# Kernel optimization log

Measured on AMD Instinct MI355X. Metric: run time of the kernel, lower is better.

## Reference

```python
import jax, jax.numpy as jnp
import numpy as np

N = 100000
E = 1600000
IN_C = 128
HID_C = 32
HEADS = 4
OUT_C = 64
NUM_CLASSES = 2
NUM_GRAPHS = 64
NEG_SLOPE = 0.2  # PyG GATConv default leaky_relu slope


def _segment_softmax(logits, seg, num_segments):
    # logits: [E, H], seg: [E] destination node ids
    m = jax.ops.segment_max(logits, seg, num_segments=num_segments)
    m = jnp.where(jnp.isfinite(m), m, 0.0)
    e = jnp.exp(logits - m[seg])
    s = jax.ops.segment_sum(e, seg, num_segments=num_segments)
    return e / (s[seg] + 1e-16)


def _gat_conv(x, src, dst, W, att_src, att_dst, bias, heads, ch, concat):
    n = x.shape[0]
    h = (x @ W).reshape(n, heads, ch)                 # [N, H, C]
    a_src = jnp.sum(h * att_src, axis=-1)             # [N, H]
    a_dst = jnp.sum(h * att_dst, axis=-1)             # [N, H]
    alpha = jax.nn.leaky_relu(a_src[src] + a_dst[dst], NEG_SLOPE)  # [E, H]
    alpha = _segment_softmax(alpha, dst, n)
    msg = h[src] * alpha[:, :, None]                  # [E, H, C]
    out = jax.ops.segment_sum(msg, dst, num_segments=n)  # [N, H, C]
    out = out.reshape(n, heads * ch) if concat else out.mean(axis=1)
    return out + bias


def setup_inputs() -> dict:
    key = jax.random.key(0)
    ks = jax.random.split(key, 12)
    x = jax.random.normal(ks[0], (N, IN_C), dtype=jnp.float32)
    edge_index = jax.random.randint(ks[1], (2, E), 0, N, dtype=jnp.int32)
    batch = jnp.sort(jax.random.randint(ks[2], (N,), 0, NUM_GRAPHS, dtype=jnp.int32))
    s1 = 1.0 / np.sqrt(IN_C)
    W1 = jax.random.uniform(ks[3], (IN_C, HEADS * HID_C), minval=-s1, maxval=s1, dtype=jnp.float32)
    att_src1 = jax.random.normal(ks[4], (HEADS, HID_C), dtype=jnp.float32) * 0.1
    att_dst1 = jax.random.normal(ks[5], (HEADS, HID_C), dtype=jnp.float32) * 0.1
    b1 = jnp.zeros((HEADS * HID_C,), dtype=jnp.float32)
    s2 = 1.0 / np.sqrt(HEADS * HID_C)
    W2 = jax.random.uniform(ks[6], (HEADS * HID_C, OUT_C), minval=-s2, maxval=s2, dtype=jnp.float32)
    att_src2 = jax.random.normal(ks[7], (1, OUT_C), dtype=jnp.float32) * 0.1
    att_dst2 = jax.random.normal(ks[8], (1, OUT_C), dtype=jnp.float32) * 0.1
    b2 = jnp.zeros((OUT_C,), dtype=jnp.float32)
    sc = 1.0 / np.sqrt(OUT_C)
    Wc = jax.random.uniform(ks[9], (OUT_C, NUM_CLASSES), minval=-sc, maxval=sc, dtype=jnp.float32)
    bc = jnp.zeros((NUM_CLASSES,), dtype=jnp.float32)
    return {"x": x, "edge_index": edge_index, "batch": batch,
            "W1": W1, "att_src1": att_src1, "att_dst1": att_dst1, "b1": b1,
            "W2": W2, "att_src2": att_src2, "att_dst2": att_dst2, "b2": b2,
            "Wc": Wc, "bc": bc}


def reference(x, edge_index, batch, W1, att_src1, att_dst1, b1,
              W2, att_src2, att_dst2, b2, Wc, bc):
    # PyG GATConv adds self-loops by default
    loops = jnp.arange(N, dtype=edge_index.dtype)
    src = jnp.concatenate([edge_index[0], loops])
    dst = jnp.concatenate([edge_index[1], loops])
    # eval mode: dropout is identity
    h = _gat_conv(x, src, dst, W1, att_src1, att_dst1, b1, HEADS, HID_C, True)
    h = jax.nn.elu(h)
    h = _gat_conv(h, src, dst, W2, att_src2, att_dst2, b2, 1, OUT_C, False)
    h = jax.nn.elu(h)
    # global mean pool over graphs
    sums = jax.ops.segment_sum(h, batch, num_segments=NUM_GRAPHS)
    cnts = jax.ops.segment_sum(jnp.ones((N, 1), h.dtype), batch, num_segments=NUM_GRAPHS)
    pooled = sums / jnp.maximum(cnts, 1.0)
    return pooled @ Wc + bc
```

## Files before the change

kernel.cpp:

```cpp
#include <hip/hip_runtime.h>
#include <math.h>


typedef __attribute__((ext_vector_type(8))) short bf16x8;
typedef __attribute__((ext_vector_type(4))) float f32x4;

__device__ __forceinline__ unsigned f2bf_rne(float x){
  unsigned u = __float_as_uint(x);
  return (u + 0x7fffu + ((u >> 16) & 1u)) >> 16;
}
__device__ __forceinline__ unsigned pk_bf2(float a, float b){
  return f2bf_rne(a) | (f2bf_rne(b) << 16);
}
__device__ __forceinline__ void unpack8(uint4 q, float* f){
  f[0] = __uint_as_float(q.x << 16);
  f[1] = __uint_as_float(q.x & 0xffff0000u);
  f[2] = __uint_as_float(q.y << 16);
  f[3] = __uint_as_float(q.y & 0xffff0000u);
  f[4] = __uint_as_float(q.z << 16);
  f[5] = __uint_as_float(q.z & 0xffff0000u);
  f[6] = __uint_as_float(q.w << 16);
  f[7] = __uint_as_float(q.w & 0xffff0000u);
}


#define CHUNKE 2048

__global__ __launch_bounds__(256) void k_bucketcount(
    const int* __restrict__ dst, int* __restrict__ bcnt, int e, int NB)
{
  __shared__ int hcnt[512];
  const int tid = threadIdx.x;
  for (int b = tid; b < 512; b += 256) hcnt[b] = 0;
  __syncthreads();
  const int lo = blockIdx.x * CHUNKE;
  const int hi = min(lo + CHUNKE, e);
  for (int i = lo + tid; i < hi; i += 256)
    atomicAdd(&hcnt[dst[i] >> 8], 1);
  __syncthreads();
  for (int b = tid; b < NB; b += 256)
    if (hcnt[b]) atomicAdd(&bcnt[b], hcnt[b]);
}

__global__ __launch_bounds__(512) void k_bucketscan(
    const int* __restrict__ bcnt, int* __restrict__ bbase,
    int* __restrict__ cur, int* __restrict__ off, int e, int n, int NB)
{
  __shared__ int sh[512];
  const int t = threadIdx.x;
  int v = (t < NB) ? bcnt[t] : 0;
  sh[t] = v;
  __syncthreads();
  for (int o = 1; o < 512; o <<= 1){
    int x = (t >= o) ? sh[t - o] : 0;
    __syncthreads();
    sh[t] += x;
    __syncthreads();
  }
  if (t < NB){
    int excl = sh[t] - v;
    bbase[t] = excl;
    cur[t]   = excl;
  }
  if (t == 0) off[n] = e;
}

__global__ __launch_bounds__(256) void k_partition(
    const int* __restrict__ src, const int* __restrict__ dst,
    int* __restrict__ cur, unsigned* __restrict__ packed, int e, int NB)
{
  __shared__ int hcnt[512];
  __shared__ int hbase[512];
  const int tid = threadIdx.x;
  for (int b = tid; b < 512; b += 256) hcnt[b] = 0;
  __syncthreads();
  const int lo = blockIdx.x * CHUNKE;
  const int hi = min(lo + CHUNKE, e);
  for (int i = lo + tid; i < hi; i += 256)
    atomicAdd(&hcnt[dst[i] >> 8], 1);
  __syncthreads();
  for (int b = tid; b < NB; b += 256){
    int c = hcnt[b];
    hbase[b] = c ? atomicAdd(&cur[b], c) : 0;
    hcnt[b] = 0;
  }
  __syncthreads();
  for (int i = lo + tid; i < hi; i += 256){
    int d = dst[i];
    int b = d >> 8;
    int p = hbase[b] + atomicAdd(&hcnt[b], 1);
    packed[p] = (unsigned)src[i] | ((unsigned)(d & 255) << 17);
  }
}

__global__ __launch_bounds__(256) void k_bucketbuild(
    const unsigned* __restrict__ packed, const int* __restrict__ bbase,
    const int* __restrict__ bcnt, int* __restrict__ off,
    int* __restrict__ csr, int n)
{
  __shared__ int lcnt[256];
  __shared__ int loff[256];
  const int b    = blockIdx.x;
  const int tid  = threadIdx.x;
  const int seg0 = bbase[b];
  const int scnt = bcnt[b];

  lcnt[tid] = 0;
  __syncthreads();
  for (int i = tid; i < scnt; i += 256)
    atomicAdd(&lcnt[packed[seg0 + i] >> 17], 1);
  __syncthreads();
  int v = lcnt[tid];
  loff[tid] = v;
  __syncthreads();
  for (int o = 1; o < 256; o <<= 1){
    int x = (tid >= o) ? loff[tid - o] : 0;
    __syncthreads();
    loff[tid] += x;
    __syncthreads();
  }
  int excl = loff[tid] - v;
  __syncthreads();
  loff[tid] = excl;
  lcnt[tid] = 0;
  int d = (b << 8) + tid;
  if (d < n) off[d] = seg0 + excl;
  __syncthreads();
  for (int i = tid; i < scnt; i += 256){
    unsigned rec = packed[seg0 + i];
    int doff = rec >> 17;
    int s    = rec & 0x1FFFF;
    int p    = atomicAdd(&lcnt[doff], 1);
    csr[seg0 + loff[doff] + p] = s;
  }
}


template<int OUTC, int HEADS, bool XBF16, typename XT>
__global__ __launch_bounds__(256) void k_gemm_mfma(
    const XT* __restrict__ X, const float* __restrict__ W,
    const float* __restrict__ att_s, const float* __restrict__ att_d,
    unsigned short* __restrict__ H, float* __restrict__ ASRC,
    float* __restrict__ ADST, int n)
{
  constexpr int K  = 128;
  constexpr int KC = 32;
  constexpr int CT = OUTC / 16;
  constexpr int RT = 16 / CT;
  constexpr int WROWS = RT * 16;
  constexpr int BROWS = WROWS * 4;

  __shared__ unsigned short Bs[OUTC][K + 8];
  __shared__ unsigned short As[BROWS][KC + 8];

  const int tid   = threadIdx.x;
  const int lane  = tid & 63;
  const int c15   = lane & 15;
  const int quad  = lane >> 4;
  const int warow = (tid >> 6) * WROWS;
  const int row0  = blockIdx.x * BROWS;

  f32x4 acc[CT][RT];
  #pragma unroll
  for (int ct = 0; ct < CT; ++ct)
    #pragma unroll
    for (int t = 0; t < RT; ++t)
      #pragma unroll
      for (int r = 0; r < 4; ++r) acc[ct][t][r] = 0.f;

  for (int idx = tid; idx < K * OUTC / 4; idx += 256){
    int k  = idx / (OUTC / 4);
    int c4 = (idx % (OUTC / 4)) * 4;
    float4 v = *(const float4*)&W[(size_t)k * OUTC + c4];
    Bs[c4 + 0][k] = (unsigned short)f2bf_rne(v.x);
    Bs[c4 + 1][k] = (unsigned short)f2bf_rne(v.y);
    Bs[c4 + 2][k] = (unsigned short)f2bf_rne(v.z);
    Bs[c4 + 3][k] = (unsigned short)f2bf_rne(v.w);
  }

  for (int kc = 0; kc < K; kc += KC){
    if (XBF16){
      for (int idx = tid; idx < BROWS * (KC / 8); idx += 256){
        int rr = idx / (KC / 8);
        int q  = idx % (KC / 8);
        int row = row0 + rr;
        uint4 v = make_uint4(0, 0, 0, 0);
        if (row < n) v = *(const uint4*)((const unsigned short*)X + (size_t)row * K + kc + q * 8);
        *(uint4*)&As[rr][q * 8] = v;
      }
    } else {
      for (int idx = tid; idx < BROWS * (KC / 4); idx += 256){
        int rr = idx / (KC / 4);
        int q  = idx % (KC / 4);
        int row = row0 + rr;
        float4 v = make_float4(0.f, 0.f, 0.f, 0.f);
        if (row < n) v = *(const float4*)((const float*)X + (size_t)row * K + kc + q * 4);
        *(uint2*)&As[rr][q * 4] = make_uint2(pk_bf2(v.x, v.y), pk_bf2(v.z, v.w));
      }
    }
    __syncthreads();

    bf16x8 af[RT];
    #pragma unroll
    for (int t = 0; t < RT; ++t)
      af[t] = *(const bf16x8*)&As[warow + t * 16 + c15][8 * quad];
    #pragma unroll
    for (int ct = 0; ct < CT; ++ct){
      bf16x8 bfr = *(const bf16x8*)&Bs[ct * 16 + c15][kc + 8 * quad];
      #pragma unroll
      for (int t = 0; t < RT; ++t)
        acc[ct][t] = __builtin_amdgcn_mfma_f32_16x16x32_bf16(af[t], bfr, acc[ct][t], 0, 0, 0);
    }
    __syncthreads();
  }

  float ats[CT], atd[CT];
  #pragma unroll
  for (int ct = 0; ct < CT; ++ct){
    ats[ct] = att_s[ct * 16 + c15];
    atd[ct] = att_d[ct * 16 + c15];
  }
  #pragma unroll
  for (int t = 0; t < RT; ++t){
    #pragma unroll
    for (int r = 0; r < 4; ++r){
      int row = row0 + warow + t * 16 + quad * 4 + r;
      float hs[HEADS], hd[HEADS];
      #pragma unroll
      for (int h = 0; h < HEADS; ++h){ hs[h] = 0.f; hd[h] = 0.f; }
      #pragma unroll
      for (int ct = 0; ct < CT; ++ct){
        float v = acc[ct][t][r];
        constexpr int CPH = OUTC / HEADS;
        int h = (ct * 16) / CPH;
        hs[h] = fmaf(v, ats[ct], hs[h]);
        hd[h] = fmaf(v, atd[ct], hd[h]);
      }
      #pragma unroll
      for (int h = 0; h < HEADS; ++h){
        #pragma unroll
        for (int s = 1; s < 16; s <<= 1){
          hs[h] += __shfl_xor(hs[h], s);
          hd[h] += __shfl_xor(hd[h], s);
        }
      }
      if (row < n){
        #pragma unroll
        for (int ct = 0; ct < CT; ++ct)
          H[(size_t)row * OUTC + ct * 16 + c15] = (unsigned short)f2bf_rne(acc[ct][t][r]);
        if (c15 == 0){
          #pragma unroll
          for (int h = 0; h < HEADS; ++h){
            ASRC[(size_t)row * HEADS + h] = hs[h];
            ADST[(size_t)row * HEADS + h] = hd[h];
          }
        }
      }
    }
  }
}


template<int CH, int HEADS, bool OUTBF16>
__global__ __launch_bounds__(256) void k_aggregate(
    const unsigned short* __restrict__ Hmsg, const float* __restrict__ ASRC,
    const float* __restrict__ ADST, const int* __restrict__ off,
    const int* __restrict__ csr, const float* __restrict__ bias,
    void* __restrict__ OUT, int n)
{
  constexpr int CL  = CH / 8;
  constexpr int DPB = 256 / CL;
  constexpr int CPH = CH / HEADS;
  constexpr int RQ  = CH / 8;

  const int tid = threadIdx.x;
  const int ld  = tid / CL;
  const int cl  = tid % CL;
  const int c0  = cl * 8;
  const int h   = c0 / CPH;
  const int d   = blockIdx.x * DPB + ld;
  if (d >= n) return;

  const uint4* Hv = (const uint4*)Hmsg;
  const float adst = ADST[d * HEADS + h];

  float acc[8];
  float wsum;
  {
    float t = ASRC[d * HEADS + h] + adst;
    float w = __expf(fmaxf(t, 0.2f * t));
    float f[8];
    unpack8(Hv[d * RQ + cl], f);
    #pragma unroll
    for (int j = 0; j < 8; ++j) acc[j] = w * f[j];
    wsum = w;
  }

  const int s0   = off[d];
  const int cnt  = off[d + 1] - s0;
  const int full = cnt & ~7;

  for (int p = 0; p < full; p += 8){
    int idx[8];
    #pragma unroll
    for (int j = 0; j < 8; ++j) idx[j] = csr[s0 + p + j];
    float av[8];
    #pragma unroll
    for (int j = 0; j < 8; ++j) av[j] = ASRC[idx[j] * HEADS + h];
    uint4 hq[8];
    #pragma unroll
    for (int j = 0; j < 8; ++j) hq[j] = Hv[idx[j] * RQ + cl];
    #pragma unroll
    for (int j = 0; j < 8; ++j){
      float t = av[j] + adst;
      float w = __expf(fmaxf(t, 0.2f * t));
      float f[8];
      unpack8(hq[j], f);
      #pragma unroll
      for (int q = 0; q < 8; ++q) acc[q] = fmaf(w, f[q], acc[q]);
      wsum += w;
    }
  }

  const int rem = cnt - full;
  if (rem){
    int  idx[8];
    bool ok[8];
    #pragma unroll
    for (int j = 0; j < 8; ++j){
      int q = csr[s0 + full + j];
      ok[j]  = j < rem;
      idx[j] = ok[j] ? q : 0;
    }
    float av[8];
    #pragma unroll
    for (int j = 0; j < 8; ++j) av[j] = ASRC[idx[j] * HEADS + h];
    uint4 hq[8];
    #pragma unroll
    for (int j = 0; j < 8; ++j) hq[j] = Hv[idx[j] * RQ + cl];
    #pragma unroll
    for (int j = 0; j < 8; ++j){
      float t = av[j] + adst;
      float w = __expf(fmaxf(t, 0.2f * t));
      w = ok[j] ? w : 0.f;
      float f[8];
      unpack8(hq[j], f);
      #pragma unroll
      for (int q = 0; q < 8; ++q) acc[q] = fmaf(w, f[q], acc[q]);
      wsum += w;
    }
  }

  const float inv = 1.f / (wsum + 1e-16f);
  float o[8];
  #pragma unroll
  for (int j = 0; j < 8; ++j){
    float v = acc[j] * inv + bias[c0 + j];
    o[j] = v > 0.f ? v : expm1f(v);
  }
  if (OUTBF16){
    uint4 q;
    q.x = pk_bf2(o[0], o[1]); q.y = pk_bf2(o[2], o[3]);
    q.z = pk_bf2(o[4], o[5]); q.w = pk_bf2(o[6], o[7]);
    *(uint4*)((unsigned short*)OUT + (size_t)d * CH + c0) = q;
  } else {
    float* Of = (float*)OUT;
    *(float4*)&Of[(size_t)d * CH + c0 + 0] = make_float4(o[0], o[1], o[2], o[3]);
    *(float4*)&Of[(size_t)d * CH + c0 + 4] = make_float4(o[4], o[5], o[6], o[7]);
  }
}


__global__ __launch_bounds__(256) void k_pool_partial(
    const float* __restrict__ H, const int* __restrict__ batch,
    float* __restrict__ sums, int n)
{
  constexpr int CHUNK = 256;
  const int c    = threadIdx.x & 63;
  const int slot = threadIdx.x >> 6;
  const int start = blockIdx.x * CHUNK;
  const int end   = min(start + CHUNK, n);

  float acc = 0.f;
  int cur = -1;
  for (int nn = start + slot; nn < end; nn += 4){
    int g = batch[nn];
    if (g != cur){
      if (cur >= 0) atomicAdd(&sums[cur * 64 + c], acc);
      acc = 0.f; cur = g;
    }
    acc += H[(size_t)nn * 64 + c];
  }
  if (cur >= 0) atomicAdd(&sums[cur * 64 + c], acc);
}

__global__ __launch_bounds__(128) void k_classify(
    const float* __restrict__ sums, const int* __restrict__ batch,
    const float* __restrict__ Wc, const float* __restrict__ bc,
    float* __restrict__ out, int n)
{
  int t = threadIdx.x;
  if (t >= 128) return;
  int g = t >> 1, cls = t & 1;
  int lo = 0, hi = n;
  while (lo < hi){ int m = (lo + hi) >> 1; if (batch[m] < g) lo = m + 1; else hi = m; }
  int s = lo;
  lo = s; hi = n;
  while (lo < hi){ int m = (lo + hi) >> 1; if (batch[m] < g + 1) lo = m + 1; else hi = m; }
  int cnt = lo - s;
  float inv = 1.f / (float)(cnt > 1 ? cnt : 1);
  float dot = 0.f;
  #pragma unroll
  for (int c = 0; c < 64; ++c) dot = fmaf(sums[g * 64 + c], Wc[c * 2 + cls], dot);
  out[g * 2 + cls] = dot * inv + bc[cls];
}


extern "C" void kernel_launch(void* const* d_in, const int* in_sizes, int n_in,
                              void* d_out, int out_size, void* d_ws, size_t ws_size,
                              hipStream_t stream)
{
  const float* x    = (const float*)d_in[0];
  const int*   edge = (const int*)  d_in[1];
  const int*   batch= (const int*)  d_in[2];
  const float* W1   = (const float*)d_in[3];
  const float* as1w = (const float*)d_in[4];
  const float* ad1w = (const float*)d_in[5];
  const float* b1   = (const float*)d_in[6];
  const float* W2   = (const float*)d_in[7];
  const float* as2w = (const float*)d_in[8];
  const float* ad2w = (const float*)d_in[9];
  const float* b2   = (const float*)d_in[10];
  const float* Wc   = (const float*)d_in[11];
  const float* bc   = (const float*)d_in[12];

  const int n = in_sizes[2];
  const int e = in_sizes[1] / 2;
  const int* esrc = edge;
  const int* edst = edge + e;
  const int NB = (n + 255) >> 8;

  unsigned short* h1  = (unsigned short*)d_ws;
  unsigned short* h1a = h1 + (size_t)n * 128;
  float* as1 = (float*)(h1a + (size_t)n * 128);
  float* ad1 = as1 + (size_t)n * 4;
  float* as2 = ad1 + (size_t)n * 4;
  float* ad2 = as2 + (size_t)n;
  float* sums = ad2 + (size_t)n;
  int*  bcnt  = (int*)(sums + 64 * 64);
  int*  cur   = bcnt + 512;
  int*  bbase = cur + 512;
  int*  off   = bbase + 512;
  unsigned* packed = (unsigned*)(off + n + 1);
  int*  csr   = (int*)(packed + e);

  const int eb = (e + CHUNKE - 1) / CHUNKE;

  hipMemsetAsync(sums, 0, (64 * 64 + 512) * 4, stream);
  k_bucketcount<<<eb, 256, 0, stream>>>(edst, bcnt, e, NB);
  k_bucketscan <<<1, 512, 0, stream>>>(bcnt, bbase, cur, off, e, n, NB);
  k_partition  <<<eb, 256, 0, stream>>>(esrc, edst, cur, packed, e, NB);
  k_bucketbuild<<<NB, 256, 0, stream>>>(packed, bbase, bcnt, off, csr, n);

  k_gemm_mfma<128, 4, false><<<(n + 127) / 128, 256, 0, stream>>>(
      x, W1, as1w, ad1w, h1, as1, ad1, n);
  k_aggregate<128, 4, true><<<(n + 15) / 16, 256, 0, stream>>>(
      h1, as1, ad1, off, csr, b1, (void*)h1a, n);

  unsigned short* h2 = h1;
  float* h2a = (float*)h1a;
  k_gemm_mfma<64, 1, true><<<(n + 255) / 256, 256, 0, stream>>>(
      h1a, W2, as2w, ad2w, h2, as2, ad2, n);
  k_aggregate<64, 1, false><<<(n + 31) / 32, 256, 0, stream>>>(
      h2, as2, ad2, off, csr, b2, (void*)h2a, n);

  k_pool_partial<<<(n + 255) / 256, 256, 0, stream>>>(h2a, batch, sums, n);
  k_classify<<<1, 128, 0, stream>>>(sums, batch, Wc, bc, (float*)d_out, n);
}
```

Before: 384.4 us.

## Stage partitioned edges in shared memory for coalesced bucket writes

The partition kernel now uses larger edge chunks and sorts each chunk locally by bucket in LDS, using a block-level prefix scan, before writing it out. Consecutive threads then write contiguous runs into each bucket's global segment instead of scattering individual records. This targets the cost of uncoalesced scattered global stores and reduces the number of blocks doing global atomics on the bucket cursors. The price is more LDS use per block, which can lower occupancy, plus extra barriers and a 512-wide scan. The scan and the per-bucket cursor atomics assume NB is at most 512.

```diff
diff --git a/kernel.cpp b/kernel.cpp
--- a/kernel.cpp
+++ b/kernel.cpp
@@ -24,7 +24,7 @@
 }
 
 
-#define CHUNKE 2048
+#define CHUNKE 8192
 
 __global__ __launch_bounds__(256) void k_bucketcount(
     const int* __restrict__ dst, int* __restrict__ bcnt, int e, int NB)
@@ -69,27 +69,54 @@
     const int* __restrict__ src, const int* __restrict__ dst,
     int* __restrict__ cur, unsigned* __restrict__ packed, int e, int NB)
 {
+  __shared__ unsigned       recs[CHUNKE];
+  __shared__ unsigned short bkt[CHUNKE];
   __shared__ int hcnt[512];
+  __shared__ int hoff[512];
   __shared__ int hbase[512];
+
   const int tid = threadIdx.x;
-  for (int b = tid; b < 512; b += 256) hcnt[b] = 0;
-  __syncthreads();
-  const int lo = blockIdx.x * CHUNKE;
-  const int hi = min(lo + CHUNKE, e);
+  const int lo  = blockIdx.x * CHUNKE;
+  const int hi  = min(lo + CHUNKE, e);
+  const int cnt = hi - lo;
+
+  hcnt[tid] = 0; hcnt[tid + 256] = 0;
+  __syncthreads();
   for (int i = lo + tid; i < hi; i += 256)
     atomicAdd(&hcnt[dst[i] >> 8], 1);
   __syncthreads();
-  for (int b = tid; b < NB; b += 256){
-    int c = hcnt[b];
-    hbase[b] = c ? atomicAdd(&cur[b], c) : 0;
-    hcnt[b] = 0;
-  }
-  __syncthreads();
+
+  hoff[tid] = hcnt[tid]; hoff[tid + 256] = hcnt[tid + 256];
+  __syncthreads();
+  for (int o = 1; o < 512; o <<= 1){
+    int x0 = (tid >= o)       ? hoff[tid - o]       : 0;
+    int x1 = (tid + 256 >= o) ? hoff[tid + 256 - o] : 0;
+    __syncthreads();
+    hoff[tid] += x0; hoff[tid + 256] += x1;
+    __syncthreads();
+  }
+
+  int c0 = hcnt[tid], c1 = hcnt[tid + 256];
+  int e0 = hoff[tid] - c0, e1 = hoff[tid + 256] - c1;
+  hbase[tid]       = c0 ? atomicAdd(&cur[tid], c0)       : 0;
+  hbase[tid + 256] = c1 ? atomicAdd(&cur[tid + 256], c1) : 0;
+  __syncthreads();
+  hoff[tid] = e0; hoff[tid + 256] = e1;
+  hcnt[tid] = 0;  hcnt[tid + 256] = 0;
+  __syncthreads();
+
   for (int i = lo + tid; i < hi; i += 256){
     int d = dst[i];
     int b = d >> 8;
-    int p = hbase[b] + atomicAdd(&hcnt[b], 1);
-    packed[p] = (unsigned)src[i] | ((unsigned)(d & 255) << 17);
+    int p = hoff[b] + atomicAdd(&hcnt[b], 1);
+    recs[p] = (unsigned)src[i] | ((unsigned)(d & 255) << 17);
+    bkt[p]  = (unsigned short)b;
+  }
+  __syncthreads();
+
+  for (int t = tid; t < cnt; t += 256){
+    int b = bkt[t];
+    packed[hbase[b] + t - hoff[b]] = recs[t];
   }
 }
 
```

Result: faster. 376.3 us (-2.1%).
